# Optimization experiments

Measured on AMD Instinct MI355X. Metric: run time of the kernel, lower is better.

The kernel has to match this reference:

```python
import jax, jax.numpy as jnp
import numpy as np

N_NODES, N_EDGES, N_FEAT = 50000, 500000, 128
HID, LAT, N_GRAPHS = 256, 64, 512
HEADS, DH = 8, 32  # GAT: 8 heads x 32 = 256
EPS = 1e-5


def _seg_softmax(logits, seg, num):
    m = jax.ops.segment_max(logits, seg, num_segments=num)
    m = jnp.where(jnp.isfinite(m), m, 0.0)
    e = jnp.exp(logits - m[seg])
    s = jax.ops.segment_sum(e, seg, num_segments=num)
    return e / jnp.maximum(s[seg], 1e-16)


def _bn(h, g, b):  # BatchNorm1d, batch statistics
    mu = h.mean(0)
    var = h.var(0)
    return (h - mu) * jax.lax.rsqrt(var + EPS) * g + b


def _ln(h, g, b):
    mu = h.mean(-1, keepdims=True)
    var = h.var(-1, keepdims=True)
    return (h - mu) * jax.lax.rsqrt(var + EPS) * g + b


def setup_inputs() -> dict:
    key = jax.random.key(0)
    ks = iter(jax.random.split(key, 40))
    f = lambda *s: jax.random.normal(next(ks), s, dtype=jnp.float32) * 0.05
    inp = {
        'x': jax.random.normal(next(ks), (N_NODES, N_FEAT), dtype=jnp.float32),
        'W_emb': f(N_FEAT, HID), 'b_emb': f(HID),
        'W_gcn': f(HID, HID), 'b_gcn': f(HID),
        'W_gat': f(HID, HID), 'a_src': f(HEADS, DH), 'a_dst': f(HEADS, DH), 'b_gat': f(HID),
        'W_l': f(HID, HID), 'b_l': f(HID), 'W_r': f(HID, HID),
        'bn_gamma': jnp.ones((3, HID), jnp.float32), 'bn_beta': jnp.zeros((3, HID), jnp.float32),
        'Wg1': f(HID, HID // 2), 'bg1': f(HID // 2), 'Wg2': f(HID // 2, 1), 'bg2': f(1),
        'Wm1': f(HID, HID), 'bm1': f(HID), 'ln_m_g': jnp.ones(HID, jnp.float32), 'ln_m_b': jnp.zeros(HID, jnp.float32),
        'Wm2': f(HID, LAT), 'bm2': f(LAT),
        'Wv1': f(HID, HID), 'bv1': f(HID), 'ln_v_g': jnp.ones(HID, jnp.float32), 'ln_v_b': jnp.zeros(HID, jnp.float32),
        'Wv2': f(HID, LAT), 'bv2': f(LAT),
        'edge_index': jax.random.randint(next(ks), (2, N_EDGES), 0, N_NODES, dtype=jnp.int64),
        'batch': jnp.sort(jax.random.randint(next(ks), (N_NODES,), 0, N_GRAPHS, dtype=jnp.int64)),
    }
    return inp


def _forward(x, W_emb, b_emb, W_gcn, b_gcn, W_gat, a_src, a_dst, b_gat,
             W_l, b_l, W_r, bn_gamma, bn_beta, Wg1, bg1, Wg2, bg2,
             Wm1, bm1, ln_m_g, ln_m_b, Wm2, bm2, Wv1, bv1, ln_v_g, ln_v_b, Wv2, bv2,
             edge_index, batch):
    N = x.shape[0]
    loops = jnp.arange(N)
    src_sl = jnp.concatenate([edge_index[0], loops])  # with self-loops (GCN/GAT)
    dst_sl = jnp.concatenate([edge_index[1], loops])

    h = x @ W_emb + b_emb  # [N, HID]

    # --- layer 0: GCNConv ---
    deg = jax.ops.segment_sum(jnp.ones_like(dst_sl, dtype=h.dtype), dst_sl, num_segments=N)
    dis = jax.lax.rsqrt(deg)
    norm = dis[src_sl] * dis[dst_sl]  # [E+N]
    xt = h @ W_gcn
    out = jax.ops.segment_sum(xt[src_sl] * norm[:, None], dst_sl, num_segments=N) + b_gcn
    out = jax.nn.relu(_bn(out, bn_gamma[0], bn_beta[0]))
    h = h + out

    # --- layer 1: GATConv (8 heads, concat) ---
    xt = (h @ W_gat).reshape(N, HEADS, DH)
    al_src = (xt * a_src).sum(-1)  # [N, H]
    al_dst = (xt * a_dst).sum(-1)
    logits = jax.nn.leaky_relu(al_src[src_sl] + al_dst[dst_sl], 0.2)  # [E+N, H]
    alpha = _seg_softmax(logits, dst_sl, N)
    out = jax.ops.segment_sum(xt[src_sl] * alpha[:, :, None], dst_sl, num_segments=N)
    out = out.reshape(N, HID) + b_gat
    out = jax.nn.relu(_bn(out, bn_gamma[1], bn_beta[1]))
    h = h + out

    # --- layer 2: SAGEConv (mean aggregation, no self-loops) ---
    src, dst = edge_index[0], edge_index[1]
    cnt = jax.ops.segment_sum(jnp.ones_like(dst, dtype=h.dtype), dst, num_segments=N)
    nb_mean = jax.ops.segment_sum(h[src], dst, num_segments=N) / jnp.maximum(cnt, 1.0)[:, None]
    out = nb_mean @ W_l + b_l + h @ W_r
    out = jax.nn.relu(_bn(out, bn_gamma[2], bn_beta[2]))
    h = h + out

    # --- GlobalAttention pooling ---
    gate = (jax.nn.relu(h @ Wg1 + bg1) @ Wg2 + bg2)[:, 0]  # [N]
    w = _seg_softmax(gate, batch, N_GRAPHS)
    h_graph = jax.ops.segment_sum(h * w[:, None], batch, num_segments=N_GRAPHS)  # [G, HID]

    mu = jax.nn.relu(_ln(h_graph @ Wm1 + bm1, ln_m_g, ln_m_b)) @ Wm2 + bm2
    logvar = jax.nn.relu(_ln(h_graph @ Wv1 + bv1, ln_v_g, ln_v_b)) @ Wv2 + bv2
    return mu, logvar


def reference(x, W_emb, b_emb, W_gcn, b_gcn, W_gat, a_src, a_dst, b_gat,
              W_l, b_l, W_r, bn_gamma, bn_beta, Wg1, bg1, Wg2, bg2,
              Wm1, bm1, ln_m_g, ln_m_b, Wm2, bm2, Wv1, bv1, ln_v_g, ln_v_b, Wv2, bv2,
              edge_index, batch):
    return _forward(x, W_emb, b_emb, W_gcn, b_gcn, W_gat, a_src, a_dst, b_gat,
                    W_l, b_l, W_r, bn_gamma, bn_beta, Wg1, bg1, Wg2, bg2,
                    Wm1, bm1, ln_m_g, ln_m_b, Wm2, bm2, Wv1, bv1, ln_v_g, ln_v_b, Wv2, bv2,
                    edge_index, batch)
```

## Files before the change

kernel.cpp:

```cpp
#include <hip/hip_runtime.h>
#include <cstdint>
#include <cstddef>

#define N_NODES 50000
#define N_EDGES 500000
#define NG 512
#define HID 256
#define EPS 1e-5f
#define SCB 49

typedef __attribute__((ext_vector_type(8))) __bf16 bf16x8;
typedef __attribute__((ext_vector_type(8))) ushort u16x8;
typedef __attribute__((ext_vector_type(4))) float f32x4;

__device__ __forceinline__ ushort f2bf(float f) {
  uint32_t u = __float_as_uint(f);
  uint32_t r = (u + 0x7fffu + ((u >> 16) & 1u)) >> 16;
  return (ushort)r;
}
__device__ __forceinline__ float bfu(ushort u) { return __uint_as_float(((uint32_t)u) << 16); }
__device__ __forceinline__ float4 bf4(ushort4 u) {
  return make_float4(bfu(u.x), bfu(u.y), bfu(u.z), bfu(u.w));
}

__global__ void k_csr_count(const int* __restrict__ ei, int* __restrict__ cnt) {
  int e = blockIdx.x * 256 + threadIdx.x;
  if (e < N_EDGES) atomicAdd(&cnt[ei[N_EDGES + e]], 1);
}

__global__ void k_scan_part(const int* __restrict__ cnt, int* __restrict__ psum) {
  __shared__ int red[256];
  int tid = threadIdx.x;
  int i0 = blockIdx.x * 1024 + tid * 4;
  int s = 0;
  if (i0 + 4 <= N_NODES) {
    int4 v = *reinterpret_cast<const int4*>(cnt + i0);
    s = v.x + v.y + v.z + v.w;
  } else {
    for (int k = 0; k < 4; k++)
      if (i0 + k < N_NODES) s += cnt[i0 + k];
  }
  red[tid] = s;
  __syncthreads();
  for (int o = 128; o > 0; o >>= 1) {
    if (tid < o) red[tid] += red[tid + o];
    __syncthreads();
  }
  if (tid == 0) psum[blockIdx.x] = red[0];
}

__global__ void k_scan_top(const int* __restrict__ psum, int* __restrict__ boff,
                           int* __restrict__ row_ptr) {
  int t = threadIdx.x;
  int v = (t < SCB) ? psum[t] : 0;
  int own = v;
  for (int o = 1; o < 64; o <<= 1) {
    int u = __shfl_up(v, o);
    if (t >= o) v += u;
  }
  if (t < SCB) boff[t] = v - own;
  if (t == 63) row_ptr[N_NODES] = v;
}

__global__ void k_scan_out(const int* __restrict__ cnt, const int* __restrict__ boff,
                           int* __restrict__ row_ptr, float* __restrict__ dis) {
  __shared__ int ps[256];
  int tid = threadIdx.x;
  int i0 = blockIdx.x * 1024 + tid * 4;
  int v[4];
#pragma unroll
  for (int k = 0; k < 4; k++) v[k] = (i0 + k < N_NODES) ? cnt[i0 + k] : 0;
  int s = v[0] + v[1] + v[2] + v[3];
  ps[tid] = s;
  __syncthreads();
  for (int o = 1; o < 256; o <<= 1) {
    int add = (tid >= o) ? ps[tid - o] : 0;
    __syncthreads();
    ps[tid] += add;
    __syncthreads();
  }
  int run = boff[blockIdx.x] + ((tid > 0) ? ps[tid - 1] : 0);
#pragma unroll
  for (int k = 0; k < 4; k++) {
    if (i0 + k < N_NODES) {
      row_ptr[i0 + k] = run;
      dis[i0 + k] = rsqrtf((float)v[k] + 1.0f);
      run += v[k];
    }
  }
}

__global__ void k_csr_fill(const int* __restrict__ ei, const int* __restrict__ row_ptr,
                           int* __restrict__ fill, int* __restrict__ col_src) {
  int e = blockIdx.x * 256 + threadIdx.x;
  if (e >= N_EDGES) return;
  int s = ei[e], d = ei[N_EDGES + e];
  int pos = row_ptr[d] + atomicAdd(&fill[d], 1);
  col_src[pos] = s;
}

struct WtArgs {
  const float* src[6];
  ushort* dst[6];
  int K[6];
  int C[6];
  int off[6];
};

__global__ void k_wt_all(WtArgs a) {
  int b = blockIdx.x;
  int ji = 0;
#pragma unroll
  for (int t = 1; t < 6; t++)
    if (b >= a.off[t]) ji = t;
  int K = a.K[ji], C = a.C[ji];
  int i = (b - a.off[ji]) * 256 + threadIdx.x;
  int c = i / K, k = i - c * K;
  a.dst[ji][i] = f2bf(a.src[ji][k * C + c]);
}

template <int K, int C, bool DUAL, bool AFP32, bool GATE>
__global__ __launch_bounds__(256) void k_mgemm(
    const void* __restrict__ A1v, const ushort* __restrict__ W1t,
    const ushort* __restrict__ A2, const ushort* __restrict__ W2t,
    const float* __restrict__ bias, float* __restrict__ out,
    ushort* __restrict__ out_bf, const float* __restrict__ gw,
    const float* __restrict__ gb, float* __restrict__ gate, int M, int relu) {
  constexpr int KS = K / 32;
  constexpr int CHK = K / 8;
  constexpr int NPAN = C / 64;
  __shared__ ushort wlds[64 * K];
  const int tid = threadIdx.x;
  const int lane = tid & 63;
  const int wid = tid >> 6;
  const int r16 = lane & 15;
  const int kg = lane >> 4;
  const int rbase = blockIdx.x * 64 + wid * 16;

  int arow = rbase + r16;
  if (arow >= M) arow = M - 1;

  bf16x8 af[KS], af2[KS];
  if constexpr (AFP32) {
    const float* ap = (const float*)A1v + (size_t)arow * K + kg * 8;
#pragma unroll
    for (int ks = 0; ks < KS; ks++) {
      float4 lo = *reinterpret_cast<const float4*>(ap + ks * 32);
      float4 hi = *reinterpret_cast<const float4*>(ap + ks * 32 + 4);
      union { u16x8 u; bf16x8 b; } cv;
      cv.u = (u16x8){f2bf(lo.x), f2bf(lo.y), f2bf(lo.z), f2bf(lo.w),
                     f2bf(hi.x), f2bf(hi.y), f2bf(hi.z), f2bf(hi.w)};
      af[ks] = cv.b;
    }
  } else {
    const ushort* ap = (const ushort*)A1v + (size_t)arow * K + kg * 8;
#pragma unroll
    for (int ks = 0; ks < KS; ks++)
      af[ks] = *reinterpret_cast<const bf16x8*>(ap + ks * 32);
  }
  if constexpr (DUAL) {
    const ushort* ap = A2 + (size_t)arow * K + kg * 8;
#pragma unroll
    for (int ks = 0; ks < KS; ks++)
      af2[ks] = *reinterpret_cast<const bf16x8*>(ap + ks * 32);
  }

  float greg[4] = {0.f, 0.f, 0.f, 0.f};

#define STAGE(WT)                                                              \
  {                                                                            \
    _Pragma("unroll") for (int jj = 0; jj < (64 * CHK) / 256; jj++) {          \
      int ci = jj * 256 + tid;                                                 \
      int c = ci / CHK, k16 = ci % CHK;                                        \
      int slot = c * CHK + (k16 ^ (c & 7));                                    \
      *reinterpret_cast<float4*>(&wlds[slot * 8]) =                            \
          *reinterpret_cast<const float4*>(&(WT)[(size_t)(c0 + c) * K + k16 * 8]); \
    }                                                                          \
  }

#define COMPUTE(AF)                                                            \
  {                                                                            \
    _Pragma("unroll") for (int ct = 0; ct < 4; ct++) {                         \
      bf16x8 wf[KS];                                                           \
      int colr = ct * 16 + r16;                                                \
      _Pragma("unroll") for (int ks = 0; ks < KS; ks++) {                      \
        int slot = colr * CHK + ((ks * 4 + kg) ^ (r16 & 7));                   \
        wf[ks] = *reinterpret_cast<const bf16x8*>(&wlds[slot * 8]);            \
      }                                                                        \
      _Pragma("unroll") for (int ks = 0; ks < KS; ks++)                        \
        acc[ct] = __builtin_amdgcn_mfma_f32_16x16x32_bf16((AF)[ks], wf[ks],    \
                                                          acc[ct], 0, 0, 0);   \
    }                                                                          \
  }

#pragma unroll
  for (int pan = 0; pan < NPAN; pan++) {
    const int c0 = pan * 64;
    f32x4 acc[4];
#pragma unroll
    for (int ct = 0; ct < 4; ct++) acc[ct] = (f32x4){0.f, 0.f, 0.f, 0.f};

    if (pan) __syncthreads();
    STAGE(W1t);
    __syncthreads();
    COMPUTE(af);
    if constexpr (DUAL) {
      __syncthreads();
      STAGE(W2t);
      __syncthreads();
      COMPUTE(af2);
    }

    if constexpr (GATE) {
#pragma unroll
      for (int ct = 0; ct < 4; ct++) {
        int col = c0 + ct * 16 + r16;
        float bv = bias[col];
        float wv = gw[col];
#pragma unroll
        for (int i = 0; i < 4; i++) {
          float v = fmaxf(acc[ct][i] + bv, 0.f);
          greg[i] = fmaf(v, wv, greg[i]);
        }
      }
    } else {
#pragma unroll
      for (int ct = 0; ct < 4; ct++) {
        int col = c0 + ct * 16 + r16;
        float bv = bias ? bias[col] : 0.f;
#pragma unroll
        for (int i = 0; i < 4; i++) {
          int row = rbase + kg * 4 + i;
          if (row < M) {
            float v = acc[ct][i] + bv;
            if (relu) v = fmaxf(v, 0.f);
            if (out) out[(size_t)row * C + col] = v;
            if (out_bf) out_bf[(size_t)row * C + col] = f2bf(v);
          }
        }
      }
    }
  }

  if constexpr (GATE) {
#pragma unroll
    for (int i = 0; i < 4; i++) {
#pragma unroll
      for (int o = 1; o < 16; o <<= 1) greg[i] += __shfl_xor(greg[i], o);
    }
    if (r16 == 0) {
      float b0 = gb[0];
#pragma unroll
      for (int i = 0; i < 4; i++) {
        int row = rbase + kg * 4 + i;
        if (row < M) gate[row] = greg[i] + b0;
      }
    }
  }
#undef STAGE
#undef COMPUTE
}

__global__ void k_gcn_agg(const ushort* __restrict__ xt, const float* __restrict__ dis,
                          const int* __restrict__ row_ptr, const int* __restrict__ col_src,
                          const float* __restrict__ b_gcn, float* __restrict__ out) {
  int node = blockIdx.x * 4 + (threadIdx.x >> 6);
  if (node >= N_NODES) return;
  int lane = threadIdx.x & 63;
  float di = dis[node];
  float4 x = bf4(*reinterpret_cast<const ushort4*>(xt + (size_t)node * HID + lane * 4));
  float w0 = di * di;
  float4 acc = make_float4(x.x * w0, x.y * w0, x.z * w0, x.w * w0);
  int b = row_ptr[node], e = row_ptr[node + 1];
  int i = b;
  for (; i + 4 <= e; i += 4) {
    int s0 = col_src[i], s1 = col_src[i + 1], s2 = col_src[i + 2], s3 = col_src[i + 3];
    ushort4 u0 = *reinterpret_cast<const ushort4*>(xt + (size_t)s0 * HID + lane * 4);
    ushort4 u1 = *reinterpret_cast<const ushort4*>(xt + (size_t)s1 * HID + lane * 4);
    ushort4 u2 = *reinterpret_cast<const ushort4*>(xt + (size_t)s2 * HID + lane * 4);
    ushort4 u3 = *reinterpret_cast<const ushort4*>(xt + (size_t)s3 * HID + lane * 4);
    float n0 = di * dis[s0], n1 = di * dis[s1], n2 = di * dis[s2], n3 = di * dis[s3];
    float4 v0 = bf4(u0), v1 = bf4(u1), v2 = bf4(u2), v3 = bf4(u3);
    acc.x = fmaf(v0.x, n0, acc.x); acc.y = fmaf(v0.y, n0, acc.y);
    acc.z = fmaf(v0.z, n0, acc.z); acc.w = fmaf(v0.w, n0, acc.w);
    acc.x = fmaf(v1.x, n1, acc.x); acc.y = fmaf(v1.y, n1, acc.y);
    acc.z = fmaf(v1.z, n1, acc.z); acc.w = fmaf(v1.w, n1, acc.w);
    acc.x = fmaf(v2.x, n2, acc.x); acc.y = fmaf(v2.y, n2, acc.y);
    acc.z = fmaf(v2.z, n2, acc.z); acc.w = fmaf(v2.w, n2, acc.w);
    acc.x = fmaf(v3.x, n3, acc.x); acc.y = fmaf(v3.y, n3, acc.y);
    acc.z = fmaf(v3.z, n3, acc.z); acc.w = fmaf(v3.w, n3, acc.w);
  }
  for (; i < e; i++) {
    int s = col_src[i];
    float nw = di * dis[s];
    float4 xv = bf4(*reinterpret_cast<const ushort4*>(xt + (size_t)s * HID + lane * 4));
    acc.x = fmaf(xv.x, nw, acc.x); acc.y = fmaf(xv.y, nw, acc.y);
    acc.z = fmaf(xv.z, nw, acc.z); acc.w = fmaf(xv.w, nw, acc.w);
  }
  float4 bb = *reinterpret_cast<const float4*>(b_gcn + lane * 4);
  acc.x += bb.x; acc.y += bb.y; acc.z += bb.z; acc.w += bb.w;
  *reinterpret_cast<float4*>(out + (size_t)node * HID + lane * 4) = acc;
}

__global__ void k_gat_al(const ushort* __restrict__ xt, const float* __restrict__ a_src,
                         const float* __restrict__ a_dst, float* __restrict__ alsrc,
                         float* __restrict__ aldst) {
  int node = blockIdx.x * 4 + (threadIdx.x >> 6);
  if (node >= N_NODES) return;
  int lane = threadIdx.x & 63;
  float4 v = bf4(*reinterpret_cast<const ushort4*>(xt + (size_t)node * HID + lane * 4));
  float4 as = *reinterpret_cast<const float4*>(a_src + lane * 4);
  float4 ad = *reinterpret_cast<const float4*>(a_dst + lane * 4);
  float ps = v.x * as.x + v.y * as.y + v.z * as.z + v.w * as.w;
  float pd = v.x * ad.x + v.y * ad.y + v.z * ad.z + v.w * ad.w;
  for (int o = 1; o < 8; o <<= 1) { ps += __shfl_xor(ps, o); pd += __shfl_xor(pd, o); }
  if ((lane & 7) == 0) {
    alsrc[node * 8 + (lane >> 3)] = ps;
    aldst[node * 8 + (lane >> 3)] = pd;
  }
}

__device__ __forceinline__ float leaky02(float x) { return x > 0.f ? x : 0.2f * x; }

__global__ void k_gat_agg(const ushort* __restrict__ xt, const float* __restrict__ alsrc,
                          const float* __restrict__ aldst, const int* __restrict__ row_ptr,
                          const int* __restrict__ col_src, const float* __restrict__ b_gat,
                          float* __restrict__ out) {
  int node = blockIdx.x * 4 + (threadIdx.x >> 6);
  if (node >= N_NODES) return;
  int lane = threadIdx.x & 63;
  int hh = lane >> 3;
  float ad = aldst[node * 8 + hh];
  float e0 = __expf(leaky02(alsrc[node * 8 + hh] + ad));
  float4 x = bf4(*reinterpret_cast<const ushort4*>(xt + (size_t)node * HID + lane * 4));
  float4 acc = make_float4(x.x * e0, x.y * e0, x.z * e0, x.w * e0);
  float s = e0;
  int b = row_ptr[node], e = row_ptr[node + 1];
  int i = b;
  for (; i + 4 <= e; i += 4) {
    int s0 = col_src[i], s1 = col_src[i + 1], s2 = col_src[i + 2], s3 = col_src[i + 3];
    float g0 = alsrc[s0 * 8 + hh], g1 = alsrc[s1 * 8 + hh];
    float g2 = alsrc[s2 * 8 + hh], g3 = alsrc[s3 * 8 + hh];
    ushort4 u0 = *reinterpret_cast<const ushort4*>(xt + (size_t)s0 * HID + lane * 4);
    ushort4 u1 = *reinterpret_cast<const ushort4*>(xt + (size_t)s1 * HID + lane * 4);
    ushort4 u2 = *reinterpret_cast<const ushort4*>(xt + (size_t)s2 * HID + lane * 4);
    ushort4 u3 = *reinterpret_cast<const ushort4*>(xt + (size_t)s3 * HID + lane * 4);
    float a1 = __expf(leaky02(g0 + ad));
    float a2 = __expf(leaky02(g1 + ad));
    float a3 = __expf(leaky02(g2 + ad));
    float a4 = __expf(leaky02(g3 + ad));
    s += a1 + a2 + a3 + a4;
    float4 v0 = bf4(u0), v1 = bf4(u1), v2 = bf4(u2), v3 = bf4(u3);
    acc.x = fmaf(v0.x, a1, acc.x); acc.y = fmaf(v0.y, a1, acc.y);
    acc.z = fmaf(v0.z, a1, acc.z); acc.w = fmaf(v0.w, a1, acc.w);
    acc.x = fmaf(v1.x, a2, acc.x); acc.y = fmaf(v1.y, a2, acc.y);
    acc.z = fmaf(v1.z, a2, acc.z); acc.w = fmaf(v1.w, a2, acc.w);
    acc.x = fmaf(v2.x, a3, acc.x); acc.y = fmaf(v2.y, a3, acc.y);
    acc.z = fmaf(v2.z, a3, acc.z); acc.w = fmaf(v2.w, a3, acc.w);
    acc.x = fmaf(v3.x, a4, acc.x); acc.y = fmaf(v3.y, a4, acc.y);
    acc.z = fmaf(v3.z, a4, acc.z); acc.w = fmaf(v3.w, a4, acc.w);
  }
  for (; i < e; i++) {
    int src = col_src[i];
    float al = __expf(leaky02(alsrc[src * 8 + hh] + ad));
    s += al;
    float4 xv = bf4(*reinterpret_cast<const ushort4*>(xt + (size_t)src * HID + lane * 4));
    acc.x = fmaf(xv.x, al, acc.x); acc.y = fmaf(xv.y, al, acc.y);
    acc.z = fmaf(xv.z, al, acc.z); acc.w = fmaf(xv.w, al, acc.w);
  }
  float inv_s = 1.0f / s;
  float4 bb = *reinterpret_cast<const float4*>(b_gat + lane * 4);
  acc.x = fmaf(acc.x, inv_s, bb.x);
  acc.y = fmaf(acc.y, inv_s, bb.y);
  acc.z = fmaf(acc.z, inv_s, bb.z);
  acc.w = fmaf(acc.w, inv_s, bb.w);
  *reinterpret_cast<float4*>(out + (size_t)node * HID + lane * 4) = acc;
}

__global__ void k_sage_agg(const ushort* __restrict__ h, const int* __restrict__ row_ptr,
                           const int* __restrict__ col_src, ushort* __restrict__ out) {
  int node = blockIdx.x * 4 + (threadIdx.x >> 6);
  if (node >= N_NODES) return;
  int lane = threadIdx.x & 63;
  int b = row_ptr[node], e = row_ptr[node + 1];
  float inv = 1.0f / fmaxf((float)(e - b), 1.0f);
  float4 acc = make_float4(0.f, 0.f, 0.f, 0.f);
  int i = b;
  for (; i + 4 <= e; i += 4) {
    int s0 = col_src[i], s1 = col_src[i + 1], s2 = col_src[i + 2], s3 = col_src[i + 3];
    ushort4 u0 = *reinterpret_cast<const ushort4*>(h + (size_t)s0 * HID + lane * 4);
    ushort4 u1 = *reinterpret_cast<const ushort4*>(h + (size_t)s1 * HID + lane * 4);
    ushort4 u2 = *reinterpret_cast<const ushort4*>(h + (size_t)s2 * HID + lane * 4);
    ushort4 u3 = *reinterpret_cast<const ushort4*>(h + (size_t)s3 * HID + lane * 4);
    float4 v0 = bf4(u0), v1 = bf4(u1), v2 = bf4(u2), v3 = bf4(u3);
    acc.x += v0.x + v1.x + v2.x + v3.x;
    acc.y += v0.y + v1.y + v2.y + v3.y;
    acc.z += v0.z + v1.z + v2.z + v3.z;
    acc.w += v0.w + v1.w + v2.w + v3.w;
  }
  for (; i < e; i++) {
    int s = col_src[i];
    float4 xv = bf4(*reinterpret_cast<const ushort4*>(h + (size_t)s * HID + lane * 4));
    acc.x += xv.x; acc.y += xv.y; acc.z += xv.z; acc.w += xv.w;
  }
  *reinterpret_cast<ushort4*>(out + (size_t)node * HID + lane * 4) =
      make_ushort4(f2bf(acc.x * inv), f2bf(acc.y * inv), f2bf(acc.z * inv), f2bf(acc.w * inv));
}

__global__ void k_bn_stats(const float* __restrict__ x, float* __restrict__ stats) {
  int c = threadIdx.x;
  float s = 0.f, q = 0.f;
  for (int r = blockIdx.x; r < N_NODES; r += gridDim.x) {
    float v = x[(size_t)r * HID + c];
    s += v;
    q = fmaf(v, v, q);
  }
  atomicAdd(&stats[c], s);
  atomicAdd(&stats[HID + c], q);
}

__global__ void k_bn_apply(const float* __restrict__ x, const float* __restrict__ stats,
                           const float* __restrict__ gamma, const float* __restrict__ beta,
                           float* __restrict__ h, ushort* __restrict__ h_bf) {
  const float invN = 1.0f / (float)N_NODES;
  int total = N_NODES * 64;
  for (int i = blockIdx.x * 256 + threadIdx.x; i < total; i += gridDim.x * 256) {
    int c4 = (i & 63) * 4;
    float4 xv = *reinterpret_cast<const float4*>(x + (size_t)i * 4);
    float4 sm = *reinterpret_cast<const float4*>(stats + c4);
    float4 sq = *reinterpret_cast<const float4*>(stats + HID + c4);
    float4 gm = *reinterpret_cast<const float4*>(gamma + c4);
    float4 bt = *reinterpret_cast<const float4*>(beta + c4);
    float4 hv = *reinterpret_cast<const float4*>(h + (size_t)i * 4);
#define BN1(f)                                                    \
  {                                                               \
    float mu = sm.f * invN;                                       \
    float var = sq.f * invN - mu * mu;                            \
    float sc = gm.f * rsqrtf(var + EPS);                          \
    float v = (xv.f - mu) * sc + bt.f;                            \
    hv.f += fmaxf(v, 0.f);                                        \
  }
    BN1(x) BN1(y) BN1(z) BN1(w)
#undef BN1
    *reinterpret_cast<float4*>(h + (size_t)i * 4) = hv;
    *reinterpret_cast<ushort4*>(h_bf + (size_t)i * 4) =
        make_ushort4(f2bf(hv.x), f2bf(hv.y), f2bf(hv.z), f2bf(hv.w));
  }
}

__global__ void k_gstart(const int* __restrict__ batch, int* __restrict__ gstart) {
  int g = blockIdx.x * 256 + threadIdx.x;
  if (g > NG) return;
  int lo = 0, hi = N_NODES;
  while (lo < hi) {
    int mid = (lo + hi) >> 1;
    if (batch[mid] < g) lo = mid + 1; else hi = mid;
  }
  gstart[g] = lo;
}

__global__ void k_pool(const float* __restrict__ h, const float* __restrict__ gate,
                       const int* __restrict__ gstart, float* __restrict__ hg) {
  __shared__ float red[256];
  __shared__ float wbuf[256];
  int g = blockIdx.x, tid = threadIdx.x;
  int b = gstart[g], e = gstart[g + 1];
  float m = -1e30f;
  for (int r = b + tid; r < e; r += 256) m = fmaxf(m, gate[r]);
  red[tid] = m;
  __syncthreads();
  for (int o = 128; o > 0; o >>= 1) {
    if (tid < o) red[tid] = fmaxf(red[tid], red[tid + o]);
    __syncthreads();
  }
  m = red[0];
  __syncthreads();
  float s = 0.f;
  for (int r = b + tid; r < e; r += 256) s += __expf(gate[r] - m);
  red[tid] = s;
  __syncthreads();
  for (int o = 128; o > 0; o >>= 1) {
    if (tid < o) red[tid] += red[tid + o];
    __syncthreads();
  }
  float inv = 1.0f / fmaxf(red[0], 1e-16f);
  __syncthreads();
  float acc = 0.f;
  for (int cb = b; cb < e; cb += 256) {
    int r = cb + tid;
    wbuf[tid] = (r < e) ? __expf(gate[r] - m) : 0.f;
    __syncthreads();
    int n = min(256, e - cb);
    for (int j = 0; j < n; j++) acc = fmaf(h[(size_t)(cb + j) * HID + tid], wbuf[j], acc);
    __syncthreads();
  }
  hg[(size_t)g * HID + tid] = acc * inv;
}

__global__ void k_mlp(const float* __restrict__ hg, const float* __restrict__ W1,
                      const float* __restrict__ b1, const float* __restrict__ lng,
                      const float* __restrict__ lnb, const float* __restrict__ W2,
                      const float* __restrict__ b2, float* __restrict__ out) {
  __shared__ float row[HID];
  __shared__ float z[HID];
  __shared__ float red[HID];
  int g = blockIdx.x, tid = threadIdx.x;
  row[tid] = hg[(size_t)g * HID + tid];
  __syncthreads();
  float acc = b1[tid];
  for (int k = 0; k < HID; k++) acc = fmaf(row[k], W1[(size_t)k * HID + tid], acc);
  red[tid] = acc;
  __syncthreads();
  for (int o = 128; o > 0; o >>= 1) {
    if (tid < o) red[tid] += red[tid + o];
    __syncthreads();
  }
  float mu = red[0] * (1.0f / HID);
  __syncthreads();
  red[tid] = acc * acc;
  __syncthreads();
  for (int o = 128; o > 0; o >>= 1) {
    if (tid < o) red[tid] += red[tid + o];
    __syncthreads();
  }
  float var = red[0] * (1.0f / HID) - mu * mu;
  float zz = (acc - mu) * rsqrtf(var + EPS) * lng[tid] + lnb[tid];
  z[tid] = fmaxf(zz, 0.f);
  __syncthreads();
  if (tid < 64) {
    float o = b2[tid];
    for (int k = 0; k < HID; k++) o = fmaf(z[k], W2[(size_t)k * 64 + tid], o);
    out[(size_t)g * 64 + tid] = o;
  }
}

extern "C" void kernel_launch(void* const* d_in, const int* in_sizes, int n_in,
                              void* d_out, int out_size, void* d_ws, size_t ws_size,
                              hipStream_t stream) {
  const float* x     = (const float*)d_in[0];
  const float* W_emb = (const float*)d_in[1];
  const float* b_emb = (const float*)d_in[2];
  const float* W_gcn = (const float*)d_in[3];
  const float* b_gcn = (const float*)d_in[4];
  const float* W_gat = (const float*)d_in[5];
  const float* a_src = (const float*)d_in[6];
  const float* a_dst = (const float*)d_in[7];
  const float* b_gat = (const float*)d_in[8];
  const float* W_l   = (const float*)d_in[9];
  const float* b_l   = (const float*)d_in[10];
  const float* W_r   = (const float*)d_in[11];
  const float* bn_g  = (const float*)d_in[12];
  const float* bn_b  = (const float*)d_in[13];
  const float* Wg1   = (const float*)d_in[14];
  const float* bg1   = (const float*)d_in[15];
  const float* Wg2   = (const float*)d_in[16];
  const float* bg2   = (const float*)d_in[17];
  const float* Wm1   = (const float*)d_in[18];
  const float* bm1   = (const float*)d_in[19];
  const float* lnmg  = (const float*)d_in[20];
  const float* lnmb  = (const float*)d_in[21];
  const float* Wm2   = (const float*)d_in[22];
  const float* bm2   = (const float*)d_in[23];
  const float* Wv1   = (const float*)d_in[24];
  const float* bv1   = (const float*)d_in[25];
  const float* lnvg  = (const float*)d_in[26];
  const float* lnvb  = (const float*)d_in[27];
  const float* Wv2   = (const float*)d_in[28];
  const float* bv2   = (const float*)d_in[29];
  const int* ei      = (const int*)d_in[30];
  const int* batch   = (const int*)d_in[31];
  float* out = (float*)d_out;

  float* ws = (float*)d_ws;
  float* h     = ws;
  float* t1    = h + (size_t)N_NODES * HID;
  float* alsrc = t1 + (size_t)N_NODES * HID;
  float* aldst = alsrc + N_NODES * 8;
  float* dis   = aldst + N_NODES * 8;
  float* gate  = dis + N_NODES;
  float* hg    = gate + N_NODES;
  float* zbase = hg + NG * HID;
  float* bnst  = zbase;
  int* row_cnt = (int*)(zbase + 3 * 512);
  int* fill    = row_cnt + N_NODES;
  int* row_ptr = fill + N_NODES;
  int* col_src = row_ptr + N_NODES + 1;
  int* gstart  = col_src + N_EDGES;
  int* psum    = gstart + NG + 1;
  int* boff    = psum + 64;

  size_t off = (size_t)((char*)(boff + 64) - (char*)d_ws);
  off = (off + 15) & ~(size_t)15;
  ushort* h_bf   = (ushort*)((char*)d_ws + off);
  ushort* t0_bf  = h_bf + (size_t)N_NODES * HID;
  ushort* wemb_t = t0_bf + (size_t)N_NODES * HID;
  ushort* wgcn_t = wemb_t + 128 * 256;
  ushort* wgat_t = wgcn_t + 256 * 256;
  ushort* wr_t   = wgat_t + 256 * 256;
  ushort* wl_t   = wr_t + 256 * 256;
  ushort* wg1_t  = wl_t + 256 * 256;

  size_t zbytes = (size_t)3 * 512 * 4 + 2 * (size_t)N_NODES * 4;
  hipMemsetAsync(zbase, 0, zbytes, stream);

  k_csr_count<<<(N_EDGES + 255) / 256, 256, 0, stream>>>(ei, row_cnt);
  k_scan_part<<<SCB, 256, 0, stream>>>(row_cnt, psum);
  k_scan_top<<<1, 64, 0, stream>>>(psum, boff, row_ptr);
  k_scan_out<<<SCB, 256, 0, stream>>>(row_cnt, boff, row_ptr, dis);
  k_csr_fill<<<(N_EDGES + 255) / 256, 256, 0, stream>>>(ei, row_ptr, fill, col_src);

  WtArgs wa;
  wa.src[0] = W_emb; wa.dst[0] = wemb_t; wa.K[0] = 128; wa.C[0] = 256; wa.off[0] = 0;
  wa.src[1] = W_gcn; wa.dst[1] = wgcn_t; wa.K[1] = 256; wa.C[1] = 256; wa.off[1] = 128;
  wa.src[2] = W_gat; wa.dst[2] = wgat_t; wa.K[2] = 256; wa.C[2] = 256; wa.off[2] = 384;
  wa.src[3] = W_r;   wa.dst[3] = wr_t;   wa.K[3] = 256; wa.C[3] = 256; wa.off[3] = 640;
  wa.src[4] = W_l;   wa.dst[4] = wl_t;   wa.K[4] = 256; wa.C[4] = 256; wa.off[4] = 896;
  wa.src[5] = Wg1;   wa.dst[5] = wg1_t;  wa.K[5] = 256; wa.C[5] = 128; wa.off[5] = 1152;
  k_wt_all<<<1280, 256, 0, stream>>>(wa);

  const int RB = (N_NODES + 63) / 64;
  const int AB = (N_NODES + 3) / 4;

  k_mgemm<128, 256, false, true, false><<<RB, 256, 0, stream>>>(
      x, wemb_t, nullptr, nullptr, b_emb, h, h_bf, nullptr, nullptr, nullptr, N_NODES, 0);

  k_mgemm<256, 256, false, false, false><<<RB, 256, 0, stream>>>(
      h_bf, wgcn_t, nullptr, nullptr, nullptr, nullptr, t0_bf, nullptr, nullptr, nullptr, N_NODES, 0);
  k_gcn_agg<<<AB, 256, 0, stream>>>(t0_bf, dis, row_ptr, col_src, b_gcn, t1);
  k_bn_stats<<<256, 256, 0, stream>>>(t1, bnst);
  k_bn_apply<<<1024, 256, 0, stream>>>(t1, bnst, bn_g, bn_b, h, h_bf);

  k_mgemm<256, 256, false, false, false><<<RB, 256, 0, stream>>>(
      h_bf, wgat_t, nullptr, nullptr, nullptr, nullptr, t0_bf, nullptr, nullptr, nullptr, N_NODES, 0);
  k_gat_al<<<AB, 256, 0, stream>>>(t0_bf, a_src, a_dst, alsrc, aldst);
  k_gat_agg<<<AB, 256, 0, stream>>>(t0_bf, alsrc, aldst, row_ptr, col_src, b_gat, t1);
  k_bn_stats<<<256, 256, 0, stream>>>(t1, bnst + 512);
  k_bn_apply<<<1024, 256, 0, stream>>>(t1, bnst + 512, bn_g + HID, bn_b + HID, h, h_bf);

  k_sage_agg<<<AB, 256, 0, stream>>>(h_bf, row_ptr, col_src, t0_bf);
  k_mgemm<256, 256, true, false, false><<<RB, 256, 0, stream>>>(
      h_bf, wr_t, t0_bf, wl_t, b_l, t1, nullptr, nullptr, nullptr, nullptr, N_NODES, 0);
  k_bn_stats<<<256, 256, 0, stream>>>(t1, bnst + 1024);
  k_bn_apply<<<1024, 256, 0, stream>>>(t1, bnst + 1024, bn_g + 2 * HID, bn_b + 2 * HID, h, h_bf);

  k_mgemm<256, 128, false, false, true><<<RB, 256, 0, stream>>>(
      h_bf, wg1_t, nullptr, nullptr, bg1, nullptr, nullptr, Wg2, bg2, gate, N_NODES, 1);
  k_gstart<<<3, 256, 0, stream>>>(batch, gstart);
  k_pool<<<NG, 256, 0, stream>>>(h, gate, gstart, hg);

  k_mlp<<<NG, 256, 0, stream>>>(hg, Wm1, bm1, lnmg, lnmb, Wm2, bm2, out);
  k_mlp<<<NG, 256, 0, stream>>>(hg, Wv1, bv1, lnvg, lnvb, Wv2, bv2, out + (size_t)NG * 64);
}
```

Before: 672.4 us.

## Store aggregation outputs in bf16 and split edges across wave halves

The GCN, GAT and SAGE aggregation kernels now write their pre-BatchNorm outputs as bf16 instead of fp32, and the BN stats and apply kernels read bf16. Pooling reads the bf16 copy of h. Each wave now has its two 32-lane halves process alternate edge pairs with 16-byte loads, then combine their partial sums with a cross-half shuffle. This halves intermediate memory traffic and increases memory-level parallelism in the gathers, at the cost of extra rounding before BatchNorm and pooling.

```diff
diff --git a/kernel.cpp b/kernel.cpp
--- a/kernel.cpp
+++ b/kernel.cpp
@@ -263,43 +263,57 @@
 
 __global__ void k_gcn_agg(const ushort* __restrict__ xt, const float* __restrict__ dis,
                           const int* __restrict__ row_ptr, const int* __restrict__ col_src,
-                          const float* __restrict__ b_gcn, float* __restrict__ out) {
+                          const float* __restrict__ b_gcn, ushort* __restrict__ outb) {
   int node = blockIdx.x * 4 + (threadIdx.x >> 6);
   if (node >= N_NODES) return;
   int lane = threadIdx.x & 63;
+  int half = lane >> 5;
+  int c0 = (lane & 31) * 8;
   float di = dis[node];
-  float4 x = bf4(*reinterpret_cast<const ushort4*>(xt + (size_t)node * HID + lane * 4));
-  float w0 = di * di;
-  float4 acc = make_float4(x.x * w0, x.y * w0, x.z * w0, x.w * w0);
+  float acc[8];
+#pragma unroll
+  for (int j = 0; j < 8; j++) acc[j] = 0.f;
   int b = row_ptr[node], e = row_ptr[node + 1];
-  int i = b;
-  for (; i + 4 <= e; i += 4) {
-    int s0 = col_src[i], s1 = col_src[i + 1], s2 = col_src[i + 2], s3 = col_src[i + 3];
-    ushort4 u0 = *reinterpret_cast<const ushort4*>(xt + (size_t)s0 * HID + lane * 4);
-    ushort4 u1 = *reinterpret_cast<const ushort4*>(xt + (size_t)s1 * HID + lane * 4);
-    ushort4 u2 = *reinterpret_cast<const ushort4*>(xt + (size_t)s2 * HID + lane * 4);
-    ushort4 u3 = *reinterpret_cast<const ushort4*>(xt + (size_t)s3 * HID + lane * 4);
-    float n0 = di * dis[s0], n1 = di * dis[s1], n2 = di * dis[s2], n3 = di * dis[s3];
-    float4 v0 = bf4(u0), v1 = bf4(u1), v2 = bf4(u2), v3 = bf4(u3);
-    acc.x = fmaf(v0.x, n0, acc.x); acc.y = fmaf(v0.y, n0, acc.y);
-    acc.z = fmaf(v0.z, n0, acc.z); acc.w = fmaf(v0.w, n0, acc.w);
-    acc.x = fmaf(v1.x, n1, acc.x); acc.y = fmaf(v1.y, n1, acc.y);
-    acc.z = fmaf(v1.z, n1, acc.z); acc.w = fmaf(v1.w, n1, acc.w);
-    acc.x = fmaf(v2.x, n2, acc.x); acc.y = fmaf(v2.y, n2, acc.y);
-    acc.z = fmaf(v2.z, n2, acc.z); acc.w = fmaf(v2.w, n2, acc.w);
-    acc.x = fmaf(v3.x, n3, acc.x); acc.y = fmaf(v3.y, n3, acc.y);
-    acc.z = fmaf(v3.z, n3, acc.z); acc.w = fmaf(v3.w, n3, acc.w);
-  }
-  for (; i < e; i++) {
-    int s = col_src[i];
-    float nw = di * dis[s];
-    float4 xv = bf4(*reinterpret_cast<const ushort4*>(xt + (size_t)s * HID + lane * 4));
-    acc.x = fmaf(xv.x, nw, acc.x); acc.y = fmaf(xv.y, nw, acc.y);
-    acc.z = fmaf(xv.z, nw, acc.z); acc.w = fmaf(xv.w, nw, acc.w);
-  }
-  float4 bb = *reinterpret_cast<const float4*>(b_gcn + lane * 4);
-  acc.x += bb.x; acc.y += bb.y; acc.z += bb.z; acc.w += bb.w;
-  *reinterpret_cast<float4*>(out + (size_t)node * HID + lane * 4) = acc;
+  int g0 = b;
+  for (; g0 + 4 <= e; g0 += 4) {
+    int i0 = g0 + half * 2;
+    int s0 = col_src[i0], s1 = col_src[i0 + 1];
+    float w0 = di * dis[s0], w1 = di * dis[s1];
+    u16x8 u0 = *reinterpret_cast<const u16x8*>(xt + (size_t)s0 * HID + c0);
+    u16x8 u1 = *reinterpret_cast<const u16x8*>(xt + (size_t)s1 * HID + c0);
+#pragma unroll
+    for (int j = 0; j < 8; j++) {
+      acc[j] = fmaf(bfu(u0[j]), w0, acc[j]);
+      acc[j] = fmaf(bfu(u1[j]), w1, acc[j]);
+    }
+  }
+  {
+    int i0 = g0 + half * 2;
+    int s0 = 0, s1 = 0;
+    float w0 = 0.f, w1 = 0.f;
+    if (i0 < e) { s0 = col_src[i0]; w0 = di * dis[s0]; }
+    if (i0 + 1 < e) { s1 = col_src[i0 + 1]; w1 = di * dis[s1]; }
+    u16x8 u0 = *reinterpret_cast<const u16x8*>(xt + (size_t)s0 * HID + c0);
+    u16x8 u1 = *reinterpret_cast<const u16x8*>(xt + (size_t)s1 * HID + c0);
+#pragma unroll
+    for (int j = 0; j < 8; j++) {
+      acc[j] = fmaf(bfu(u0[j]), w0, acc[j]);
+      acc[j] = fmaf(bfu(u1[j]), w1, acc[j]);
+    }
+  }
+#pragma unroll
+  for (int j = 0; j < 8; j++) acc[j] += __shfl_xor(acc[j], 32);
+  if (!half) {
+    u16x8 un = *reinterpret_cast<const u16x8*>(xt + (size_t)node * HID + c0);
+    float w0 = di * di;
+    u16x8 r;
+#pragma unroll
+    for (int j = 0; j < 8; j++) {
+      float v = fmaf(bfu(un[j]), w0, acc[j]) + b_gcn[c0 + j];
+      r[j] = f2bf(v);
+    }
+    *reinterpret_cast<u16x8*>(outb + (size_t)node * HID + c0) = r;
+  }
 }
 
 __global__ void k_gat_al(const ushort* __restrict__ xt, const float* __restrict__ a_src,
@@ -325,93 +339,117 @@
 __global__ void k_gat_agg(const ushort* __restrict__ xt, const float* __restrict__ alsrc,
                           const float* __restrict__ aldst, const int* __restrict__ row_ptr,
                           const int* __restrict__ col_src, const float* __restrict__ b_gat,
-                          float* __restrict__ out) {
+                          ushort* __restrict__ outb) {
   int node = blockIdx.x * 4 + (threadIdx.x >> 6);
   if (node >= N_NODES) return;
   int lane = threadIdx.x & 63;
-  int hh = lane >> 3;
+  int half = lane >> 5;
+  int l32 = lane & 31;
+  int c0 = l32 * 8;
+  int hh = l32 >> 2;
   float ad = aldst[node * 8 + hh];
-  float e0 = __expf(leaky02(alsrc[node * 8 + hh] + ad));
-  float4 x = bf4(*reinterpret_cast<const ushort4*>(xt + (size_t)node * HID + lane * 4));
-  float4 acc = make_float4(x.x * e0, x.y * e0, x.z * e0, x.w * e0);
-  float s = e0;
+  float acc[8];
+#pragma unroll
+  for (int j = 0; j < 8; j++) acc[j] = 0.f;
+  float s = 0.f;
   int b = row_ptr[node], e = row_ptr[node + 1];
-  int i = b;
-  for (; i + 4 <= e; i += 4) {
-    int s0 = col_src[i], s1 = col_src[i + 1], s2 = col_src[i + 2], s3 = col_src[i + 3];
-    float g0 = alsrc[s0 * 8 + hh], g1 = alsrc[s1 * 8 + hh];
-    float g2 = alsrc[s2 * 8 + hh], g3 = alsrc[s3 * 8 + hh];
-    ushort4 u0 = *reinterpret_cast<const ushort4*>(xt + (size_t)s0 * HID + lane * 4);
-    ushort4 u1 = *reinterpret_cast<const ushort4*>(xt + (size_t)s1 * HID + lane * 4);
-    ushort4 u2 = *reinterpret_cast<const ushort4*>(xt + (size_t)s2 * HID + lane * 4);
-    ushort4 u3 = *reinterpret_cast<const ushort4*>(xt + (size_t)s3 * HID + lane * 4);
-    float a1 = __expf(leaky02(g0 + ad));
-    float a2 = __expf(leaky02(g1 + ad));
-    float a3 = __expf(leaky02(g2 + ad));
-    float a4 = __expf(leaky02(g3 + ad));
-    s += a1 + a2 + a3 + a4;
-    float4 v0 = bf4(u0), v1 = bf4(u1), v2 = bf4(u2), v3 = bf4(u3);
-    acc.x = fmaf(v0.x, a1, acc.x); acc.y = fmaf(v0.y, a1, acc.y);
-    acc.z = fmaf(v0.z, a1, acc.z); acc.w = fmaf(v0.w, a1, acc.w);
-    acc.x = fmaf(v1.x, a2, acc.x); acc.y = fmaf(v1.y, a2, acc.y);
-    acc.z = fmaf(v1.z, a2, acc.z); acc.w = fmaf(v1.w, a2, acc.w);
-    acc.x = fmaf(v2.x, a3, acc.x); acc.y = fmaf(v2.y, a3, acc.y);
-    acc.z = fmaf(v2.z, a3, acc.z); acc.w = fmaf(v2.w, a3, acc.w);
-    acc.x = fmaf(v3.x, a4, acc.x); acc.y = fmaf(v3.y, a4, acc.y);
-    acc.z = fmaf(v3.z, a4, acc.z); acc.w = fmaf(v3.w, a4, acc.w);
-  }
-  for (; i < e; i++) {
-    int src = col_src[i];
-    float al = __expf(leaky02(alsrc[src * 8 + hh] + ad));
-    s += al;
-    float4 xv = bf4(*reinterpret_cast<const ushort4*>(xt + (size_t)src * HID + lane * 4));
-    acc.x = fmaf(xv.x, al, acc.x); acc.y = fmaf(xv.y, al, acc.y);
-    acc.z = fmaf(xv.z, al, acc.z); acc.w = fmaf(xv.w, al, acc.w);
-  }
-  float inv_s = 1.0f / s;
-  float4 bb = *reinterpret_cast<const float4*>(b_gat + lane * 4);
-  acc.x = fmaf(acc.x, inv_s, bb.x);
-  acc.y = fmaf(acc.y, inv_s, bb.y);
-  acc.z = fmaf(acc.z, inv_s, bb.z);
-  acc.w = fmaf(acc.w, inv_s, bb.w);
-  *reinterpret_cast<float4*>(out + (size_t)node * HID + lane * 4) = acc;
+  int g0 = b;
+  for (; g0 + 4 <= e; g0 += 4) {
+    int i0 = g0 + half * 2;
+    int s0 = col_src[i0], s1 = col_src[i0 + 1];
+    float a0 = __expf(leaky02(alsrc[s0 * 8 + hh] + ad));
+    float a1 = __expf(leaky02(alsrc[s1 * 8 + hh] + ad));
+    u16x8 u0 = *reinterpret_cast<const u16x8*>(xt + (size_t)s0 * HID + c0);
+    u16x8 u1 = *reinterpret_cast<const u16x8*>(xt + (size_t)s1 * HID + c0);
+    s += a0 + a1;
+#pragma unroll
+    for (int j = 0; j < 8; j++) {
+      acc[j] = fmaf(bfu(u0[j]), a0, acc[j]);
+      acc[j] = fmaf(bfu(u1[j]), a1, acc[j]);
+    }
+  }
+  {
+    int i0 = g0 + half * 2;
+    int s0 = 0, s1 = 0;
+    float a0 = 0.f, a1 = 0.f;
+    if (i0 < e) { s0 = col_src[i0]; a0 = __expf(leaky02(alsrc[s0 * 8 + hh] + ad)); }
+    if (i0 + 1 < e) { s1 = col_src[i0 + 1]; a1 = __expf(leaky02(alsrc[s1 * 8 + hh] + ad)); }
+    u16x8 u0 = *reinterpret_cast<const u16x8*>(xt + (size_t)s0 * HID + c0);
+    u16x8 u1 = *reinterpret_cast<const u16x8*>(xt + (size_t)s1 * HID + c0);
+    s += a0 + a1;
+#pragma unroll
+    for (int j = 0; j < 8; j++) {
+      acc[j] = fmaf(bfu(u0[j]), a0, acc[j]);
+      acc[j] = fmaf(bfu(u1[j]), a1, acc[j]);
+    }
+  }
+#pragma unroll
+  for (int j = 0; j < 8; j++) acc[j] += __shfl_xor(acc[j], 32);
+  s += __shfl_xor(s, 32);
+  if (!half) {
+    float e0 = __expf(leaky02(alsrc[node * 8 + hh] + ad));
+    u16x8 un = *reinterpret_cast<const u16x8*>(xt + (size_t)node * HID + c0);
+    float inv_s = 1.0f / (s + e0);
+    u16x8 r;
+#pragma unroll
+    for (int j = 0; j < 8; j++) {
+      float v = fmaf(bfu(un[j]), e0, acc[j]) * inv_s + b_gat[c0 + j];
+      r[j] = f2bf(v);
+    }
+    *reinterpret_cast<u16x8*>(outb + (size_t)node * HID + c0) = r;
+  }
 }
 
 __global__ void k_sage_agg(const ushort* __restrict__ h, const int* __restrict__ row_ptr,
-                           const int* __restrict__ col_src, ushort* __restrict__ out) {
+                           const int* __restrict__ col_src, ushort* __restrict__ outb) {
   int node = blockIdx.x * 4 + (threadIdx.x >> 6);
   if (node >= N_NODES) return;
   int lane = threadIdx.x & 63;
+  int half = lane >> 5;
+  int c0 = (lane & 31) * 8;
+  float acc[8];
+#pragma unroll
+  for (int j = 0; j < 8; j++) acc[j] = 0.f;
   int b = row_ptr[node], e = row_ptr[node + 1];
-  float inv = 1.0f / fmaxf((float)(e - b), 1.0f);
-  float4 acc = make_float4(0.f, 0.f, 0.f, 0.f);
-  int i = b;
-  for (; i + 4 <= e; i += 4) {
-    int s0 = col_src[i], s1 = col_src[i + 1], s2 = col_src[i + 2], s3 = col_src[i + 3];
-    ushort4 u0 = *reinterpret_cast<const ushort4*>(h + (size_t)s0 * HID + lane * 4);
-    ushort4 u1 = *reinterpret_cast<const ushort4*>(h + (size_t)s1 * HID + lane * 4);
-    ushort4 u2 = *reinterpret_cast<const ushort4*>(h + (size_t)s2 * HID + lane * 4);
-    ushort4 u3 = *reinterpret_cast<const ushort4*>(h + (size_t)s3 * HID + lane * 4);
-    float4 v0 = bf4(u0), v1 = bf4(u1), v2 = bf4(u2), v3 = bf4(u3);
-    acc.x += v0.x + v1.x + v2.x + v3.x;
-    acc.y += v0.y + v1.y + v2.y + v3.y;
-    acc.z += v0.z + v1.z + v2.z + v3.z;
-    acc.w += v0.w + v1.w + v2.w + v3.w;
-  }
-  for (; i < e; i++) {
-    int s = col_src[i];
-    float4 xv = bf4(*reinterpret_cast<const ushort4*>(h + (size_t)s * HID + lane * 4));
-    acc.x += xv.x; acc.y += xv.y; acc.z += xv.z; acc.w += xv.w;
-  }
-  *reinterpret_cast<ushort4*>(out + (size_t)node * HID + lane * 4) =
-      make_ushort4(f2bf(acc.x * inv), f2bf(acc.y * inv), f2bf(acc.z * inv), f2bf(acc.w * inv));
-}
-
-__global__ void k_bn_stats(const float* __restrict__ x, float* __restrict__ stats) {
+  int g0 = b;
+  for (; g0 + 4 <= e; g0 += 4) {
+    int i0 = g0 + half * 2;
+    int s0 = col_src[i0], s1 = col_src[i0 + 1];
+    u16x8 u0 = *reinterpret_cast<const u16x8*>(h + (size_t)s0 * HID + c0);
+    u16x8 u1 = *reinterpret_cast<const u16x8*>(h + (size_t)s1 * HID + c0);
+#pragma unroll
+    for (int j = 0; j < 8; j++) acc[j] += bfu(u0[j]) + bfu(u1[j]);
+  }
+  {
+    int i0 = g0 + half * 2;
+    int s0 = 0, s1 = 0;
+    float w0 = 0.f, w1 = 0.f;
+    if (i0 < e) { s0 = col_src[i0]; w0 = 1.f; }
+    if (i0 + 1 < e) { s1 = col_src[i0 + 1]; w1 = 1.f; }
+    u16x8 u0 = *reinterpret_cast<const u16x8*>(h + (size_t)s0 * HID + c0);
+    u16x8 u1 = *reinterpret_cast<const u16x8*>(h + (size_t)s1 * HID + c0);
+#pragma unroll
+    for (int j = 0; j < 8; j++) {
+      acc[j] = fmaf(bfu(u0[j]), w0, acc[j]);
+      acc[j] = fmaf(bfu(u1[j]), w1, acc[j]);
+    }
+  }
+#pragma unroll
+  for (int j = 0; j < 8; j++) acc[j] += __shfl_xor(acc[j], 32);
+  if (!half) {
+    float inv = 1.0f / fmaxf((float)(e - b), 1.0f);
+    u16x8 r;
+#pragma unroll
+    for (int j = 0; j < 8; j++) r[j] = f2bf(acc[j] * inv);
+    *reinterpret_cast<u16x8*>(outb + (size_t)node * HID + c0) = r;
+  }
+}
+
+__global__ void k_bn_stats(const ushort* __restrict__ x, float* __restrict__ stats) {
   int c = threadIdx.x;
   float s = 0.f, q = 0.f;
   for (int r = blockIdx.x; r < N_NODES; r += gridDim.x) {
-    float v = x[(size_t)r * HID + c];
+    float v = bfu(x[(size_t)r * HID + c]);
     s += v;
     q = fmaf(v, v, q);
   }
@@ -419,14 +457,14 @@
   atomicAdd(&stats[HID + c], q);
 }
 
-__global__ void k_bn_apply(const float* __restrict__ x, const float* __restrict__ stats,
+__global__ void k_bn_apply(const ushort* __restrict__ x, const float* __restrict__ stats,
                            const float* __restrict__ gamma, const float* __restrict__ beta,
                            float* __restrict__ h, ushort* __restrict__ h_bf) {
   const float invN = 1.0f / (float)N_NODES;
   int total = N_NODES * 64;
   for (int i = blockIdx.x * 256 + threadIdx.x; i < total; i += gridDim.x * 256) {
     int c4 = (i & 63) * 4;
-    float4 xv = *reinterpret_cast<const float4*>(x + (size_t)i * 4);
+    float4 xv = bf4(*reinterpret_cast<const ushort4*>(x + (size_t)i * 4));
     float4 sm = *reinterpret_cast<const float4*>(stats + c4);
     float4 sq = *reinterpret_cast<const float4*>(stats + HID + c4);
     float4 gm = *reinterpret_cast<const float4*>(gamma + c4);
@@ -459,7 +497,7 @@
   gstart[g] = lo;
 }
 
-__global__ void k_pool(const float* __restrict__ h, const float* __restrict__ gate,
+__global__ void k_pool(const ushort* __restrict__ hb, const float* __restrict__ gate,
                        const int* __restrict__ gstart, float* __restrict__ hg) {
   __shared__ float red[256];
   __shared__ float wbuf[256];
@@ -491,7 +529,8 @@
     wbuf[tid] = (r < e) ? __expf(gate[r] - m) : 0.f;
     __syncthreads();
     int n = min(256, e - cb);
-    for (int j = 0; j < n; j++) acc = fmaf(h[(size_t)(cb + j) * HID + tid], wbuf[j], acc);
+    for (int j = 0; j < n; j++)
+      acc = fmaf(bfu(hb[(size_t)(cb + j) * HID + tid]), wbuf[j], acc);
     __syncthreads();
   }
   hg[(size_t)g * HID + tid] = acc * inv;
@@ -589,6 +628,8 @@
   int* psum    = gstart + NG + 1;
   int* boff    = psum + 64;
 
+  ushort* t1b = (ushort*)t1;
+
   size_t off = (size_t)((char*)(boff + 64) - (char*)d_ws);
   off = (off + 15) & ~(size_t)15;
   ushort* h_bf   = (ushort*)((char*)d_ws + off);
@@ -626,27 +667,27 @@
 
   k_mgemm<256, 256, false, false, false><<<RB, 256, 0, stream>>>(
       h_bf, wgcn_t, nullptr, nullptr, nullptr, nullptr, t0_bf, nullptr, nullptr, nullptr, N_NODES, 0);
-  k_gcn_agg<<<AB, 256, 0, stream>>>(t0_bf, dis, row_ptr, col_src, b_gcn, t1);
-  k_bn_stats<<<256, 256, 0, stream>>>(t1, bnst);
-  k_bn_apply<<<1024, 256, 0, stream>>>(t1, bnst, bn_g, bn_b, h, h_bf);
+  k_gcn_agg<<<AB, 256, 0, stream>>>(t0_bf, dis, row_ptr, col_src, b_gcn, t1b);
+  k_bn_stats<<<256, 256, 0, stream>>>(t1b, bnst);
+  k_bn_apply<<<1024, 256, 0, stream>>>(t1b, bnst, bn_g, bn_b, h, h_bf);
 
   k_mgemm<256, 256, false, false, false><<<RB, 256, 0, stream>>>(
       h_bf, wgat_t, nullptr, nullptr, nullptr, nullptr, t0_bf, nullptr, nullptr, nullptr, N_NODES, 0);
   k_gat_al<<<AB, 256, 0, stream>>>(t0_bf, a_src, a_dst, alsrc, aldst);
-  k_gat_agg<<<AB, 256, 0, stream>>>(t0_bf, alsrc, aldst, row_ptr, col_src, b_gat, t1);
-  k_bn_stats<<<256, 256, 0, stream>>>(t1, bnst + 512);
-  k_bn_apply<<<1024, 256, 0, stream>>>(t1, bnst + 512, bn_g + HID, bn_b + HID, h, h_bf);
+  k_gat_agg<<<AB, 256, 0, stream>>>(t0_bf, alsrc, aldst, row_ptr, col_src, b_gat, t1b);
+  k_bn_stats<<<256, 256, 0, stream>>>(t1b, bnst + 512);
+  k_bn_apply<<<1024, 256, 0, stream>>>(t1b, bnst + 512, bn_g + HID, bn_b + HID, h, h_bf);
 
   k_sage_agg<<<AB, 256, 0, stream>>>(h_bf, row_ptr, col_src, t0_bf);
   k_mgemm<256, 256, true, false, false><<<RB, 256, 0, stream>>>(
-      h_bf, wr_t, t0_bf, wl_t, b_l, t1, nullptr, nullptr, nullptr, nullptr, N_NODES, 0);
-  k_bn_stats<<<256, 256, 0, stream>>>(t1, bnst + 1024);
-  k_bn_apply<<<1024, 256, 0, stream>>>(t1, bnst + 1024, bn_g + 2 * HID, bn_b + 2 * HID, h, h_bf);
+      h_bf, wr_t, t0_bf, wl_t, b_l, nullptr, t1b, nullptr, nullptr, nullptr, N_NODES, 0);
+  k_bn_stats<<<256, 256, 0, stream>>>(t1b, bnst + 1024);
+  k_bn_apply<<<1024, 256, 0, stream>>>(t1b, bnst + 1024, bn_g + 2 * HID, bn_b + 2 * HID, h, h_bf);
 
   k_mgemm<256, 128, false, false, true><<<RB, 256, 0, stream>>>(
       h_bf, wg1_t, nullptr, nullptr, bg1, nullptr, nullptr, Wg2, bg2, gate, N_NODES, 1);
   k_gstart<<<3, 256, 0, stream>>>(batch, gstart);
-  k_pool<<<NG, 256, 0, stream>>>(h, gate, gstart, hg);
+  k_pool<<<NG, 256, 0, stream>>>(h_bf, gate, gstart, hg);
 
   k_mlp<<<NG, 256, 0, stream>>>(hg, Wm1, bm1, lnmg, lnmb, Wm2, bm2, out);
   k_mlp<<<NG, 256, 0, stream>>>(hg, Wv1, bv1, lnvg, lnvb, Wv2, bv2, out + (size_t)NG * 64);
```

After: 654.3 us. 1.03x faster.
